# Kernel optimization log

Hardware: AMD Instinct MI355X
Metric: run time of the kernel (lower is better)

Reference implementation:

```python
import jax, jax.numpy as jnp
import numpy as np

HIDDEN = 2048
N_HEADS = 32
N_KV = 8
HEAD_DIM = 128
EPS = 1e-6
THETA = 10000.0
WINDOW = 512
T = 2048


def _rms_norm(x, w, eps=EPS):
    # x: [..., d]
    var = jnp.mean(x * x, axis=-1, keepdims=True)
    return x * jax.lax.rsqrt(var + eps) * w


def _rope(x, positions):
    # neox-style full rotary, x: [T, H, d]
    d = x.shape[-1]
    inv_freq = 1.0 / (THETA ** (jnp.arange(0, d, 2, dtype=jnp.float32) / d))  # [d/2]
    ang = positions.astype(jnp.float32)[:, None] * inv_freq  # [T, d/2]
    cos = jnp.cos(ang)[:, None, :]  # [T,1,d/2]
    sin = jnp.sin(ang)[:, None, :]
    x1, x2 = x[..., : d // 2], x[..., d // 2 :]
    return jnp.concatenate([x1 * cos - x2 * sin, x2 * cos + x1 * sin], axis=-1)


def setup_inputs() -> dict:
    key = jax.random.key(0)
    ks = jax.random.split(key, 6)
    q_size = N_HEADS * HEAD_DIM
    kv_size = N_KV * HEAD_DIM
    s = 1.0 / np.sqrt(HIDDEN)
    return {
        "positions": jnp.arange(T, dtype=jnp.int32),
        "hidden_states": jax.random.normal(ks[0], (T, HIDDEN), dtype=jnp.float32),
        "w_qkv": jax.random.normal(ks[1], (HIDDEN, q_size + 2 * kv_size), dtype=jnp.float32) * s,
        "w_o": jax.random.normal(ks[2], (q_size, HIDDEN), dtype=jnp.float32) * s,
        "w_g": jax.random.normal(ks[3], (HIDDEN, N_HEADS), dtype=jnp.float32) * s,
        "q_norm_w": jnp.ones((HEAD_DIM,), dtype=jnp.float32),
        "k_norm_w": jnp.ones((HEAD_DIM,), dtype=jnp.float32),
    }


def reference(positions, hidden_states, w_qkv, w_o, w_g, q_norm_w, k_norm_w):
    t = hidden_states.shape[0]
    q_size = N_HEADS * HEAD_DIM
    kv_size = N_KV * HEAD_DIM
    scale = HEAD_DIM ** -0.5
    group = N_HEADS // N_KV

    qkv = hidden_states @ w_qkv  # [T, q+2kv]
    q = qkv[:, :q_size].reshape(t, N_HEADS, HEAD_DIM)
    k = qkv[:, q_size : q_size + kv_size].reshape(t, N_KV, HEAD_DIM)
    v = qkv[:, q_size + kv_size :].reshape(t, N_KV, HEAD_DIM)

    # per-head RMSNorm then RoPE
    q = _rope(_rms_norm(q, q_norm_w), positions)
    k = _rope(_rms_norm(k, k_norm_w), positions)

    # sliding-window causal attention with GQA (group queries per kv head)
    qg = q.reshape(t, N_KV, group, HEAD_DIM)
    scores = jnp.einsum("tkgd,skd->kgts", qg, k) * scale  # [Hkv,G,T,T]
    diff = positions[:, None] - positions[None, :]  # i - j
    mask = (diff >= 0) & (diff < WINDOW)  # causal + sliding window
    scores = jnp.where(mask[None, None], scores, -jnp.inf)
    probs = jax.nn.softmax(scores, axis=-1)
    attn = jnp.einsum("kgts,skd->tkgd", probs, v).reshape(t, N_HEADS, HEAD_DIM)

    # softplus gate per head, then output projection
    gate = jax.nn.softplus((hidden_states @ w_g).astype(jnp.float32)).astype(attn.dtype)
    attn = attn * gate[:, :, None]
    return attn.reshape(t, q_size) @ w_o
```

## Files before the change

### kernel.cpp

```cpp
#include <hip/hip_runtime.h>

typedef __attribute__((ext_vector_type(4))) float floatx4;
typedef __attribute__((ext_vector_type(8))) _Float16 half8;
typedef __attribute__((ext_vector_type(4))) _Float16 half4;

#define TT 2048
#define HIDDEN 2048
#define NH 32
#define NKV 8
#define HD 128
#define QSIZE 4096
#define KVSIZE 1024
#define QKVN 6144
#define QKVNP 6272
#define VOFF 5120
#define GOFF 6144
#define WINDOW 512

__global__ __launch_bounds__(256) void prep_kernel(
    const float* __restrict__ w_qkv, const float* __restrict__ w_o,
    const float* __restrict__ hidden, _Float16* __restrict__ Wqkvt,
    _Float16* __restrict__ Wot, _Float16* __restrict__ Xb) {
  __shared__ float tile[64][68];
  int bid = blockIdx.x;
  int tid = threadIdx.x;
  if (bid >= 5120) {
    if (bid < 7168) {
      int i = ((bid - 5120) * 256 + tid) * 8;
      float4 a = *(const float4*)&hidden[i];
      float4 b = *(const float4*)&hidden[i + 4];
      alignas(16) _Float16 o[8] = {(_Float16)a.x, (_Float16)a.y, (_Float16)a.z, (_Float16)a.w,
                                   (_Float16)b.x, (_Float16)b.y, (_Float16)b.z, (_Float16)b.w};
      *(uint4*)&Xb[i] = *(const uint4*)o;
    } else {
      int i = ((bid - 7168) * 256 + tid) * 8;
      *(uint4*)&Wqkvt[(size_t)(GOFF + NH) * HIDDEN + i] = (uint4){0, 0, 0, 0};
    }
    return;
  }
  const float* in;
  _Float16* out;
  int R, C, tilesX, t;
  if (bid < 3072) { in = w_qkv; out = Wqkvt; R = HIDDEN; C = QKVN; tilesX = 96; t = bid; }
  else           { in = w_o;   out = Wot;   R = QSIZE;  C = HIDDEN; tilesX = 32; t = bid - 3072; }
  int bc = (t % tilesX) * 64, br = (t / tilesX) * 64;
  int rr = tid >> 4, l16 = tid & 15;
#pragma unroll
  for (int it = 0; it < 4; ++it) {
    int r = rr + it * 16;
    *(float4*)&tile[r][l16 * 4] = *(const float4*)&in[(size_t)(br + r) * C + bc + l16 * 4];
  }
  __syncthreads();
  int orow = tid >> 2, rr0 = (tid & 3) * 16;
  alignas(16) _Float16 tmp[16];
#pragma unroll
  for (int jj = 0; jj < 16; ++jj) tmp[jj] = (_Float16)tile[rr0 + jj][orow];
  *(uint4*)&out[(size_t)(bc + orow) * R + br + rr0] = *(const uint4*)&tmp[0];
  *(uint4*)&out[(size_t)(bc + orow) * R + br + rr0 + 8] = *(const uint4*)&tmp[8];
}

__global__ __launch_bounds__(256) void transpose_f32_f16_kernel(
    const float* __restrict__ in, _Float16* __restrict__ out, int R, int C) {
  __shared__ float tile[32][33];
  int bc = blockIdx.x * 32;
  int br = blockIdx.y * 32;
  int c = threadIdx.x & 31;
  int r0 = threadIdx.x >> 5;
#pragma unroll
  for (int i = 0; i < 4; ++i) {
    int r = r0 + 8 * i;
    tile[r][c] = in[(size_t)(br + r) * C + bc + c];
  }
  __syncthreads();
#pragma unroll
  for (int i = 0; i < 4; ++i) {
    int r = r0 + 8 * i;
    out[(size_t)(bc + r) * R + br + c] = (_Float16)tile[c][r];
  }
}

__global__ __launch_bounds__(256) void repack_kv_kernel(const _Float16* __restrict__ Kh,
                                                        const _Float16* __restrict__ QKVh,
                                                        _Float16* __restrict__ Kf,
                                                        _Float16* __restrict__ Vf) {
  __shared__ _Float16 tile[64][136];
  int st = blockIdx.x, kh = blockIdx.y;
  int s0 = st * 64;
  if (blockIdx.z == 0) {
    _Float16* dst = Kf + (size_t)(kh * 32 + st) * 8192;
#pragma unroll
    for (int i = 0; i < 4; ++i) {
      int c = threadIdx.x + i * 256;
      int jt = c >> 8, kc = (c >> 6) & 3, quad = (c >> 4) & 3, n16 = c & 15;
      uint4 v = *(const uint4*)&Kh[((size_t)(s0 + jt * 16 + n16) * NKV + kh) * HD +
                                   kc * 32 + quad * 8];
      *(uint4*)&dst[c * 8] = v;
    }
  } else {
#pragma unroll
    for (int i = 0; i < 4; ++i) {
      int c = threadIdx.x + i * 256;
      int row = c >> 4, part = c & 15;
      *(uint4*)&tile[row][part * 8] =
          *(const uint4*)&QKVh[(size_t)(s0 + row) * QKVNP + VOFF + kh * HD + part * 8];
    }
    __syncthreads();
    _Float16* dst = Vf + (size_t)(kh * 32 + st) * 8192;
#pragma unroll
    for (int i = 0; i < 4; ++i) {
      int c = threadIdx.x + i * 256;
      int jd = c >> 7, kc = (c >> 6) & 1, quad = (c >> 4) & 3, n16 = c & 15;
      int d = jd * 16 + n16, sb = kc * 32 + quad * 8;
      alignas(16) _Float16 tmp[8];
#pragma unroll
      for (int j = 0; j < 8; ++j) tmp[j] = tile[sb + j][d];
      *(uint4*)&dst[c * 8] = *(const uint4*)tmp;
    }
  }
}

__device__ __forceinline__ void async16(const _Float16* g, _Float16* l) {
  __builtin_amdgcn_global_load_lds((const __attribute__((address_space(1))) void*)g,
                                   (__attribute__((address_space(3))) void*)l, 16, 0, 0);
}

__device__ __forceinline__ void swizzle_mn(int& m0, int& n0) {
  int ntiles = gridDim.y;
  int pid = blockIdx.x + blockIdx.y * gridDim.x;
  int band = pid / (8 * ntiles);
  int wi = pid - band * (8 * ntiles);
  m0 = (band * 8 + (wi & 7)) * 128;
  n0 = (wi >> 3) * 128;
}

template <typename OutT>
__global__ __launch_bounds__(256, 2) void gemm_bt_kernel(
    const _Float16* __restrict__ A, const _Float16* __restrict__ Bt,
    OutT* __restrict__ C, int M, int N, int K) {
  __shared__ _Float16 As[128 * 32];
  __shared__ _Float16 Bs[128 * 32];
  int tid = threadIdx.x;
  int wave = tid >> 6, lane = tid & 63;
  int wm = wave >> 1, wn = wave & 1;
  int m0, n0;
  swizzle_mn(m0, n0);
  int lr = lane & 15;
  int kq = (lane >> 4) * 8;
  floatx4 acc[4][4];
#pragma unroll
  for (int i = 0; i < 4; ++i)
#pragma unroll
    for (int j = 0; j < 4; ++j) acc[i][j] = (floatx4){0.f, 0.f, 0.f, 0.f};

  for (int k0 = 0; k0 < K; k0 += 32) {
    __syncthreads();
#pragma unroll
    for (int it = 0; it < 2; ++it) {
      int c = tid + it * 256;
      int row = c >> 2, kp = (c & 3) * 8;
      _Float16* la = &As[it * 2048 + wave * 512];
      _Float16* lb = &Bs[it * 2048 + wave * 512];
      async16(&A[(size_t)(m0 + row) * K + k0 + kp], la);
      async16(&Bt[(size_t)(n0 + row) * K + k0 + kp], lb);
    }
    __syncthreads();
    half8 a[4], b[4];
#pragma unroll
    for (int i = 0; i < 4; ++i) a[i] = *(const half8*)&As[(wm * 64 + i * 16 + lr) * 32 + kq];
#pragma unroll
    for (int j = 0; j < 4; ++j) b[j] = *(const half8*)&Bs[(wn * 64 + j * 16 + lr) * 32 + kq];
#pragma unroll
    for (int i = 0; i < 4; ++i)
#pragma unroll
      for (int j = 0; j < 4; ++j)
        acc[i][j] = __builtin_amdgcn_mfma_f32_16x16x32_f16(a[i], b[j], acc[i][j], 0, 0, 0);
  }
  int rq = (lane >> 4) * 4;
#pragma unroll
  for (int i = 0; i < 4; ++i)
#pragma unroll
    for (int j = 0; j < 4; ++j)
#pragma unroll
      for (int r = 0; r < 4; ++r) {
        int row = m0 + wm * 64 + i * 16 + rq + r;
        int col = n0 + wn * 64 + j * 16 + lr;
        C[(size_t)row * N + col] = (OutT)acc[i][j][r];
      }
}

__global__ __launch_bounds__(256, 2) void gemm_bt_splitk_kernel(
    const _Float16* __restrict__ A, const _Float16* __restrict__ Bt,
    float* __restrict__ C, int M, int N, int K, int Ks) {
  __shared__ _Float16 As[128 * 32];
  __shared__ _Float16 Bs[128 * 32];
  int tid = threadIdx.x;
  int wave = tid >> 6, lane = tid & 63;
  int wm = wave >> 1, wn = wave & 1;
  int m0, n0;
  swizzle_mn(m0, n0);
  int kb = blockIdx.z * Ks;
  int lr = lane & 15;
  int kq = (lane >> 4) * 8;
  floatx4 acc[4][4];
#pragma unroll
  for (int i = 0; i < 4; ++i)
#pragma unroll
    for (int j = 0; j < 4; ++j) acc[i][j] = (floatx4){0.f, 0.f, 0.f, 0.f};

  for (int k0 = kb; k0 < kb + Ks; k0 += 32) {
    __syncthreads();
#pragma unroll
    for (int it = 0; it < 2; ++it) {
      int c = tid + it * 256;
      int row = c >> 2, kp = (c & 3) * 8;
      _Float16* la = &As[it * 2048 + wave * 512];
      _Float16* lb = &Bs[it * 2048 + wave * 512];
      async16(&A[(size_t)(m0 + row) * K + k0 + kp], la);
      async16(&Bt[(size_t)(n0 + row) * K + k0 + kp], lb);
    }
    __syncthreads();
    half8 a[4], b[4];
#pragma unroll
    for (int i = 0; i < 4; ++i) a[i] = *(const half8*)&As[(wm * 64 + i * 16 + lr) * 32 + kq];
#pragma unroll
    for (int j = 0; j < 4; ++j) b[j] = *(const half8*)&Bs[(wn * 64 + j * 16 + lr) * 32 + kq];
#pragma unroll
    for (int i = 0; i < 4; ++i)
#pragma unroll
      for (int j = 0; j < 4; ++j)
        acc[i][j] = __builtin_amdgcn_mfma_f32_16x16x32_f16(a[i], b[j], acc[i][j], 0, 0, 0);
  }
  int rq = (lane >> 4) * 4;
#pragma unroll
  for (int i = 0; i < 4; ++i)
#pragma unroll
    for (int j = 0; j < 4; ++j)
#pragma unroll
      for (int r = 0; r < 4; ++r) {
        int row = m0 + wm * 64 + i * 16 + rq + r;
        int col = n0 + wn * 64 + j * 16 + lr;
        unsafeAtomicAdd(&C[(size_t)row * N + col], acc[i][j][r]);
      }
}

__global__ __launch_bounds__(256) void normrope_kernel(
    const _Float16* __restrict__ qkv, const float* __restrict__ qw,
    const float* __restrict__ kw, const int* __restrict__ positions,
    _Float16* __restrict__ qh, _Float16* __restrict__ khb) {
  int wid = blockIdx.x * 4 + (threadIdx.x >> 6);
  int lane = threadIdx.x & 63;
  int t, hh;
  const _Float16* src;
  _Float16* dst;
  const float* w;
  if (wid < TT * NH) {
    t = wid >> 5; hh = wid & 31;
    src = qkv + (size_t)t * QKVNP + hh * HD;
    dst = qh + ((size_t)t * NH + hh) * HD;
    w = qw;
  } else {
    int r = wid - TT * NH;
    t = r >> 3; hh = r & 7;
    src = qkv + (size_t)t * QKVNP + QSIZE + hh * HD;
    dst = khb + ((size_t)t * NKV + hh) * HD;
    w = kw;
  }
  float x1 = (float)src[lane];
  float x2 = (float)src[lane + 64];
  float ss = x1 * x1 + x2 * x2;
#pragma unroll
  for (int off = 1; off < 64; off <<= 1) ss += __shfl_xor(ss, off);
  float rr = rsqrtf(ss * (1.0f / 128.0f) + 1e-6f);
  float n1 = x1 * rr * w[lane];
  float n2 = x2 * rr * w[lane + 64];
  float pos = (float)positions[t];
  float invf = exp2f(-(float)lane * (13.287712379549449f / 64.0f));
  float ang = pos * invf;
  float sn, cs;
  sincosf(ang, &sn, &cs);
  dst[lane] = (_Float16)(n1 * cs - n2 * sn);
  dst[lane + 64] = (_Float16)(n2 * cs + n1 * sn);
}

#define PSTR 68
#define M0 8.0f
__global__ __launch_bounds__(256, 2) void attn_kernel(
    const _Float16* __restrict__ Qh, const _Float16* __restrict__ Kf,
    const _Float16* __restrict__ Vf, const _Float16* __restrict__ QKVh,
    _Float16* __restrict__ Og) {
  const float scale = 0.08838834764831845f;
  __shared__ _Float16 Ps[4][2 * 16 * PSTR];
  int tid = threadIdx.x;
  int wave = tid >> 6, lane = tid & 63;
  int n16 = lane & 15, quad = lane >> 4;
  int t0 = blockIdx.x * 32;
  int kh = blockIdx.y;
  int h = kh * 4 + wave;
  _Float16* ps = Ps[wave];

  half8 qf[2][4];
#pragma unroll
  for (int mt = 0; mt < 2; ++mt)
#pragma unroll
    for (int kc = 0; kc < 4; ++kc)
      qf[mt][kc] = *(const half8*)&Qh[((size_t)(t0 + mt * 16 + n16) * NH + h) * HD +
                                      kc * 32 + quad * 8];

  floatx4 O[2][8];
  float lp[2][4];
#pragma unroll
  for (int mt = 0; mt < 2; ++mt) {
#pragma unroll
    for (int jd = 0; jd < 8; ++jd) O[mt][jd] = (floatx4){0.f, 0.f, 0.f, 0.f};
#pragma unroll
    for (int r = 0; r < 4; ++r) lp[mt][r] = 0.f;
  }

  int lo = t0 - (WINDOW - 1);
  if (lo < 0) lo = 0;
  int st1 = (t0 + 31) >> 6;
  for (int st = lo >> 6; st <= st1; ++st) {
    int s0 = st * 64;
    const _Float16* kb = Kf + (size_t)(kh * 32 + st) * 8192;
    const _Float16* vb = Vf + (size_t)(kh * 32 + st) * 8192;
    floatx4 S[2][4];
#pragma unroll
    for (int mt = 0; mt < 2; ++mt)
#pragma unroll
      for (int jt = 0; jt < 4; ++jt) S[mt][jt] = (floatx4){0.f, 0.f, 0.f, 0.f};
#pragma unroll
    for (int jt = 0; jt < 4; ++jt) {
      half8 kfr[4];
#pragma unroll
      for (int kc = 0; kc < 4; ++kc)
        kfr[kc] = *(const half8*)&kb[(jt * 4 + kc) * 512 + lane * 8];
#pragma unroll
      for (int kc = 0; kc < 4; ++kc)
#pragma unroll
        for (int mt = 0; mt < 2; ++mt)
          S[mt][jt] = __builtin_amdgcn_mfma_f32_16x16x32_f16(qf[mt][kc], kfr[kc], S[mt][jt], 0, 0, 0);
    }
    bool interior = (t0 >= s0 + 63) && (t0 + 31 - s0 < WINDOW);
    if (interior) {
#pragma unroll
      for (int mt = 0; mt < 2; ++mt)
#pragma unroll
        for (int r = 0; r < 4; ++r) {
          float rs = 0.f;
#pragma unroll
          for (int jt = 0; jt < 4; ++jt) {
            float p = __expf(__builtin_fmaf(S[mt][jt][r], scale, -M0));
            rs += p;
            ps[(mt * 16 + quad * 4 + r) * PSTR + jt * 16 + n16] = (_Float16)p;
          }
          lp[mt][r] += rs;
        }
    } else {
#pragma unroll
      for (int mt = 0; mt < 2; ++mt)
#pragma unroll
        for (int r = 0; r < 4; ++r) {
          int tq = t0 + mt * 16 + quad * 4 + r;
          float rs = 0.f;
#pragma unroll
          for (int jt = 0; jt < 4; ++jt) {
            int diff = tq - (s0 + jt * 16 + n16);
            bool ok = (diff >= 0) && (diff < WINDOW);
            float p = ok ? __expf(__builtin_fmaf(S[mt][jt][r], scale, -M0)) : 0.f;
            rs += p;
            ps[(mt * 16 + quad * 4 + r) * PSTR + jt * 16 + n16] = (_Float16)p;
          }
          lp[mt][r] += rs;
        }
    }
    half8 pf[2][2];
#pragma unroll
    for (int mt = 0; mt < 2; ++mt)
#pragma unroll
      for (int kc = 0; kc < 2; ++kc) {
        half4 lo4 = *(const half4*)&ps[(mt * 16 + n16) * PSTR + kc * 32 + quad * 8];
        half4 hi4 = *(const half4*)&ps[(mt * 16 + n16) * PSTR + kc * 32 + quad * 8 + 4];
        pf[mt][kc] = (half8){lo4[0], lo4[1], lo4[2], lo4[3], hi4[0], hi4[1], hi4[2], hi4[3]};
      }
#pragma unroll
    for (int jd = 0; jd < 8; ++jd) {
#pragma unroll
      for (int kc = 0; kc < 2; ++kc) {
        half8 vfr = *(const half8*)&vb[(jd * 2 + kc) * 512 + lane * 8];
#pragma unroll
        for (int mt = 0; mt < 2; ++mt)
          O[mt][jd] = __builtin_amdgcn_mfma_f32_16x16x32_f16(pf[mt][kc], vfr, O[mt][jd], 0, 0, 0);
      }
    }
  }
#pragma unroll
  for (int mt = 0; mt < 2; ++mt)
#pragma unroll
    for (int r = 0; r < 4; ++r) {
      float l = lp[mt][r];
#pragma unroll
      for (int off = 1; off < 16; off <<= 1) l += __shfl_xor(l, off);
      int t = t0 + mt * 16 + quad * 4 + r;
      float gl = (float)QKVh[(size_t)t * QKVNP + GOFF + h];
      float g = (gl > 0.f) ? gl + log1pf(__expf(-gl)) : log1pf(__expf(gl));
      float inv = g / l;
#pragma unroll
      for (int jd = 0; jd < 8; ++jd)
        Og[(size_t)t * QSIZE + h * HD + jd * 16 + n16] = (_Float16)(O[mt][jd][r] * inv);
    }
}

extern "C" void kernel_launch(void* const* d_in, const int* in_sizes, int n_in,
                              void* d_out, int out_size, void* d_ws, size_t ws_size,
                              hipStream_t stream) {
  const int* positions = (const int*)d_in[0];
  const float* hidden = (const float*)d_in[1];
  const float* w_qkv = (const float*)d_in[2];
  const float* w_o = (const float*)d_in[3];
  const float* w_g = (const float*)d_in[4];
  const float* q_norm_w = (const float*)d_in[5];
  const float* k_norm_w = (const float*)d_in[6];
  float* out = (float*)d_out;

  char* ws = (char*)d_ws;
  size_t off = 0;
  auto alloc = [&](size_t bytes) {
    void* p = ws + off;
    off += (bytes + 255) & ~(size_t)255;
    return p;
  };
  _Float16* Xb = (_Float16*)alloc((size_t)TT * HIDDEN * 2);
  _Float16* Wqkvt = (_Float16*)alloc((size_t)QKVNP * HIDDEN * 2);
  _Float16* Wot = (_Float16*)alloc((size_t)HIDDEN * QSIZE * 2);
  _Float16* QKVh = (_Float16*)alloc((size_t)TT * QKVNP * 2);
  _Float16* Qh = (_Float16*)alloc((size_t)TT * NH * HD * 2);
  _Float16* Kh = (_Float16*)alloc((size_t)TT * NKV * HD * 2);
  _Float16* Kf = (_Float16*)alloc((size_t)NKV * 32 * 8192 * 2);
  _Float16* Vf = (_Float16*)alloc((size_t)NKV * 32 * 8192 * 2);
  _Float16* Og = (_Float16*)alloc((size_t)TT * QSIZE * 2);

  hipMemsetAsync(d_out, 0, (size_t)out_size * 4, stream);

  prep_kernel<<<7264, 256, 0, stream>>>(w_qkv, w_o, hidden, Wqkvt, Wot, Xb);
  transpose_f32_f16_kernel<<<dim3(1, HIDDEN / 32), 256, 0, stream>>>(
      w_g, Wqkvt + (size_t)GOFF * HIDDEN, HIDDEN, NH);
  gemm_bt_kernel<_Float16><<<dim3(TT / 128, QKVNP / 128), 256, 0, stream>>>(
      Xb, Wqkvt, QKVh, TT, QKVNP, HIDDEN);
  normrope_kernel<<<(TT * (NH + NKV)) / 4, 256, 0, stream>>>(QKVh, q_norm_w, k_norm_w,
                                                             positions, Qh, Kh);
  repack_kv_kernel<<<dim3(32, NKV, 2), 256, 0, stream>>>(Kh, QKVh, Kf, Vf);
  attn_kernel<<<dim3(TT / 32, NKV), 256, 0, stream>>>(Qh, Kf, Vf, QKVh, Og);
  gemm_bt_splitk_kernel<<<dim3(TT / 128, HIDDEN / 128, 2), 256, 0, stream>>>(
      Og, Wot, out, TT, HIDDEN, QSIZE, QSIZE / 2);
}
```

Baseline: 369.8 us.

## Double K-step to 64 in GEMMs and prefetch next K tile in attention

The two GEMM kernels now stage 64-wide K slices in shared memory, doubling LDS per block, and run two MFMA sub-steps per pair of barriers, which halves the barrier count. The attention kernel loads the next key block's fragments into registers while the softmax and PV work for the current block runs, hiding global load latency. In exchange the GEMMs use more LDS and the attention kernel holds 16 extra half8 registers, which may lower occupancy or cause spills.

```diff
diff --git a/kernel.cpp b/kernel.cpp
--- a/kernel.cpp
+++ b/kernel.cpp
@@ -137,8 +137,8 @@
 __global__ __launch_bounds__(256, 2) void gemm_bt_kernel(
     const _Float16* __restrict__ A, const _Float16* __restrict__ Bt,
     OutT* __restrict__ C, int M, int N, int K) {
-  __shared__ _Float16 As[128 * 32];
-  __shared__ _Float16 Bs[128 * 32];
+  __shared__ _Float16 As[128 * 64];
+  __shared__ _Float16 Bs[128 * 64];
   int tid = threadIdx.x;
   int wave = tid >> 6, lane = tid & 63;
   int wm = wave >> 1, wn = wave & 1;
@@ -152,28 +152,33 @@
 #pragma unroll
     for (int j = 0; j < 4; ++j) acc[i][j] = (floatx4){0.f, 0.f, 0.f, 0.f};
 
-  for (int k0 = 0; k0 < K; k0 += 32) {
+  for (int k0 = 0; k0 < K; k0 += 64) {
     __syncthreads();
 #pragma unroll
-    for (int it = 0; it < 2; ++it) {
+    for (int it = 0; it < 4; ++it) {
       int c = tid + it * 256;
-      int row = c >> 2, kp = (c & 3) * 8;
+      int row = c >> 3, kp = (c & 7) * 8;
       _Float16* la = &As[it * 2048 + wave * 512];
       _Float16* lb = &Bs[it * 2048 + wave * 512];
       async16(&A[(size_t)(m0 + row) * K + k0 + kp], la);
       async16(&Bt[(size_t)(n0 + row) * K + k0 + kp], lb);
     }
     __syncthreads();
-    half8 a[4], b[4];
-#pragma unroll
-    for (int i = 0; i < 4; ++i) a[i] = *(const half8*)&As[(wm * 64 + i * 16 + lr) * 32 + kq];
-#pragma unroll
-    for (int j = 0; j < 4; ++j) b[j] = *(const half8*)&Bs[(wn * 64 + j * 16 + lr) * 32 + kq];
-#pragma unroll
-    for (int i = 0; i < 4; ++i)
+#pragma unroll
+    for (int kc = 0; kc < 2; ++kc) {
+      half8 a[4], b[4];
+#pragma unroll
+      for (int i = 0; i < 4; ++i)
+        a[i] = *(const half8*)&As[(wm * 64 + i * 16 + lr) * 64 + kc * 32 + kq];
 #pragma unroll
       for (int j = 0; j < 4; ++j)
-        acc[i][j] = __builtin_amdgcn_mfma_f32_16x16x32_f16(a[i], b[j], acc[i][j], 0, 0, 0);
+        b[j] = *(const half8*)&Bs[(wn * 64 + j * 16 + lr) * 64 + kc * 32 + kq];
+#pragma unroll
+      for (int i = 0; i < 4; ++i)
+#pragma unroll
+        for (int j = 0; j < 4; ++j)
+          acc[i][j] = __builtin_amdgcn_mfma_f32_16x16x32_f16(a[i], b[j], acc[i][j], 0, 0, 0);
+    }
   }
   int rq = (lane >> 4) * 4;
 #pragma unroll
@@ -191,8 +196,8 @@
 __global__ __launch_bounds__(256, 2) void gemm_bt_splitk_kernel(
     const _Float16* __restrict__ A, const _Float16* __restrict__ Bt,
     float* __restrict__ C, int M, int N, int K, int Ks) {
-  __shared__ _Float16 As[128 * 32];
-  __shared__ _Float16 Bs[128 * 32];
+  __shared__ _Float16 As[128 * 64];
+  __shared__ _Float16 Bs[128 * 64];
   int tid = threadIdx.x;
   int wave = tid >> 6, lane = tid & 63;
   int wm = wave >> 1, wn = wave & 1;
@@ -207,28 +212,33 @@
 #pragma unroll
     for (int j = 0; j < 4; ++j) acc[i][j] = (floatx4){0.f, 0.f, 0.f, 0.f};
 
-  for (int k0 = kb; k0 < kb + Ks; k0 += 32) {
+  for (int k0 = kb; k0 < kb + Ks; k0 += 64) {
     __syncthreads();
 #pragma unroll
-    for (int it = 0; it < 2; ++it) {
+    for (int it = 0; it < 4; ++it) {
       int c = tid + it * 256;
-      int row = c >> 2, kp = (c & 3) * 8;
+      int row = c >> 3, kp = (c & 7) * 8;
       _Float16* la = &As[it * 2048 + wave * 512];
       _Float16* lb = &Bs[it * 2048 + wave * 512];
       async16(&A[(size_t)(m0 + row) * K + k0 + kp], la);
       async16(&Bt[(size_t)(n0 + row) * K + k0 + kp], lb);
     }
     __syncthreads();
-    half8 a[4], b[4];
-#pragma unroll
-    for (int i = 0; i < 4; ++i) a[i] = *(const half8*)&As[(wm * 64 + i * 16 + lr) * 32 + kq];
-#pragma unroll
-    for (int j = 0; j < 4; ++j) b[j] = *(const half8*)&Bs[(wn * 64 + j * 16 + lr) * 32 + kq];
-#pragma unroll
-    for (int i = 0; i < 4; ++i)
+#pragma unroll
+    for (int kc = 0; kc < 2; ++kc) {
+      half8 a[4], b[4];
+#pragma unroll
+      for (int i = 0; i < 4; ++i)
+        a[i] = *(const half8*)&As[(wm * 64 + i * 16 + lr) * 64 + kc * 32 + kq];
 #pragma unroll
       for (int j = 0; j < 4; ++j)
-        acc[i][j] = __builtin_amdgcn_mfma_f32_16x16x32_f16(a[i], b[j], acc[i][j], 0, 0, 0);
+        b[j] = *(const half8*)&Bs[(wn * 64 + j * 16 + lr) * 64 + kc * 32 + kq];
+#pragma unroll
+      for (int i = 0; i < 4; ++i)
+#pragma unroll
+        for (int j = 0; j < 4; ++j)
+          acc[i][j] = __builtin_amdgcn_mfma_f32_16x16x32_f16(a[i], b[j], acc[i][j], 0, 0, 0);
+    }
   }
   int rq = (lane >> 4) * 4;
 #pragma unroll
@@ -318,10 +328,21 @@
 
   int lo = t0 - (WINDOW - 1);
   if (lo < 0) lo = 0;
+  int st0 = lo >> 6;
   int st1 = (t0 + 31) >> 6;
-  for (int st = lo >> 6; st <= st1; ++st) {
+
+  half8 kfr[4][4];
+  {
+    const _Float16* kb = Kf + (size_t)(kh * 32 + st0) * 8192;
+#pragma unroll
+    for (int jt = 0; jt < 4; ++jt)
+#pragma unroll
+      for (int kc = 0; kc < 4; ++kc)
+        kfr[jt][kc] = *(const half8*)&kb[(jt * 4 + kc) * 512 + lane * 8];
+  }
+
+  for (int st = st0; st <= st1; ++st) {
     int s0 = st * 64;
-    const _Float16* kb = Kf + (size_t)(kh * 32 + st) * 8192;
     const _Float16* vb = Vf + (size_t)(kh * 32 + st) * 8192;
     floatx4 S[2][4];
 #pragma unroll
@@ -329,16 +350,20 @@
 #pragma unroll
       for (int jt = 0; jt < 4; ++jt) S[mt][jt] = (floatx4){0.f, 0.f, 0.f, 0.f};
 #pragma unroll
-    for (int jt = 0; jt < 4; ++jt) {
-      half8 kfr[4];
+    for (int jt = 0; jt < 4; ++jt)
 #pragma unroll
       for (int kc = 0; kc < 4; ++kc)
-        kfr[kc] = *(const half8*)&kb[(jt * 4 + kc) * 512 + lane * 8];
-#pragma unroll
-      for (int kc = 0; kc < 4; ++kc)
 #pragma unroll
         for (int mt = 0; mt < 2; ++mt)
-          S[mt][jt] = __builtin_amdgcn_mfma_f32_16x16x32_f16(qf[mt][kc], kfr[kc], S[mt][jt], 0, 0, 0);
+          S[mt][jt] = __builtin_amdgcn_mfma_f32_16x16x32_f16(qf[mt][kc], kfr[jt][kc],
+                                                             S[mt][jt], 0, 0, 0);
+    if (st < st1) {
+      const _Float16* kb = Kf + (size_t)(kh * 32 + st + 1) * 8192;
+#pragma unroll
+      for (int jt = 0; jt < 4; ++jt)
+#pragma unroll
+        for (int kc = 0; kc < 4; ++kc)
+          kfr[jt][kc] = *(const half8*)&kb[(jt * 4 + kc) * 512 + lane * 8];
     }
     bool interior = (t0 >= s0 + 63) && (t0 + 31 - s0 < WINDOW);
     if (interior) {
```

Measured after the change: 389.9 us. 5.4% more time.
